# Optimization experiments

Measured on AMD Instinct MI355X. Metric: run time of the kernel, lower is better.

Reference implementation:

```python
import jax, jax.numpy as jnp
import numpy as np

N = 50000          # nodes
E = 800000         # edges (avg degree 16)
DIN, DH, DOUT = 128, 256, 40


def setup_inputs() -> dict:
    key = jax.random.key(0)
    ks = jax.random.split(key, 6)
    x = jax.random.normal(ks[0], (N, DIN), dtype=jnp.float32)
    edge_index = jax.random.randint(ks[1], (2, E), 0, N, dtype=jnp.int32)
    W1 = jax.random.normal(ks[2], (DIN, DH), dtype=jnp.float32) * (1.0 / np.sqrt(DIN))
    b1 = jnp.zeros((DH,), dtype=jnp.float32)
    W2 = jax.random.normal(ks[3], (DH, DOUT), dtype=jnp.float32) * (1.0 / np.sqrt(DH))
    b2 = jnp.zeros((DOUT,), dtype=jnp.float32)
    return {"x": x, "edge_index": edge_index, "W1": W1, "b1": b1, "W2": W2, "b2": b2}


def gcn_conv(x, src, dst, W, b, n):
    # PyG GCNConv: add self-loops, symmetric normalization D^-1/2 A D^-1/2,
    # dense projection, scatter-sum aggregation, then bias.
    deg = jax.ops.segment_sum(jnp.ones_like(dst, dtype=x.dtype), dst, num_segments=n)
    dinv = jnp.where(deg > 0, jax.lax.rsqrt(deg), 0.0)
    norm = dinv[src] * dinv[dst]          # [E+N]
    h = x @ W                              # [N, dout] dense GEMM
    msg = h[src] * norm[:, None]          # gather + scale, [E+N, dout]
    out = jax.ops.segment_sum(msg, dst, num_segments=n)  # scatter-add
    return out + b


def reference(x, edge_index, W1, b1, W2, b2):
    n = x.shape[0]
    loops = jnp.arange(n, dtype=edge_index.dtype)
    src = jnp.concatenate([edge_index[0], loops])
    dst = jnp.concatenate([edge_index[1], loops])
    h = jax.nn.relu(gcn_conv(x, src, dst, W1, b1, n))
    h = gcn_conv(h, src, dst, W2, b2, n)
    return jax.nn.log_softmax(h, axis=1)
```

## Files before the change

### kernel.cpp

```cpp
#include <hip/hip_runtime.h>
#include <math.h>

#define DIN 128
#define DH 256
#define DOUT 40
#define MLP_ROWS 64

#define BSH 7
#define BNODES 128
#define NBUK 391
#define CAP 4096
#define PART_T 512
#define PART_EPB 8
#define PART_CHUNK (PART_T * PART_EPB)

typedef short short8 __attribute__((ext_vector_type(8)));
typedef float f32x4 __attribute__((ext_vector_type(4)));

__device__ inline unsigned f2bf(float f) {
    unsigned u = __float_as_uint(f);
    return (u + 0x7fffu + ((u >> 16) & 1u)) >> 16;
}
__device__ inline float bflo(unsigned u) { return __uint_as_float(u << 16); }
__device__ inline float bfhi(unsigned u) { return __uint_as_float(u & 0xffff0000u); }

__global__ void k_prep(const float* __restrict__ W1, const float* __restrict__ W2,
                       unsigned* __restrict__ w1t, unsigned* __restrict__ w2t,
                       int* __restrict__ gcur) {
    int i = blockIdx.x * blockDim.x + threadIdx.x;
    if (i < 256 * 64) {
        int c = i >> 6;
        int kk = (i & 63) * 2;
        w1t[i] = f2bf(W1[kk * DH + c]) | (f2bf(W1[(kk + 1) * DH + c]) << 16);
        return;
    }
    i -= 256 * 64;
    if (i < 48 * 128) {
        int col = i >> 7;
        int kk = (i & 127) * 2;
        float a = (col < DOUT) ? W2[kk * DOUT + col] : 0.f;
        float bb = (col < DOUT) ? W2[(kk + 1) * DOUT + col] : 0.f;
        w2t[i] = f2bf(a) | (f2bf(bb) << 16);
        return;
    }
    i -= 48 * 128;
    if (i < NBUK) gcur[i] = i * CAP;
}

__global__ __launch_bounds__(PART_T) void k_partition(
    const int* __restrict__ src, const int* __restrict__ dst,
    int* __restrict__ gcur, unsigned* __restrict__ raw, int E) {
    __shared__ int hist[NBUK];
    __shared__ int lbase[NBUK];
    int tid = threadIdx.x;
    int base_e = blockIdx.x * PART_CHUNK;

    for (int i = tid; i < NBUK; i += PART_T) hist[i] = 0;
    __syncthreads();

    int s[PART_EPB], d[PART_EPB];
#pragma unroll
    for (int k = 0; k < PART_EPB; ++k) {
        int e = base_e + k * PART_T + tid;
        if (e < E) { s[k] = src[e]; d[k] = dst[e]; }
        else d[k] = -1;
    }
#pragma unroll
    for (int k = 0; k < PART_EPB; ++k)
        if (d[k] >= 0) atomicAdd(&hist[d[k] >> BSH], 1);
    __syncthreads();

    for (int b = tid; b < NBUK; b += PART_T) {
        int c = hist[b];
        lbase[b] = c ? atomicAdd(&gcur[b], c) : 0;
    }
    __syncthreads();
    for (int i = tid; i < NBUK; i += PART_T) hist[i] = 0;
    __syncthreads();

#pragma unroll
    for (int k = 0; k < PART_EPB; ++k) {
        if (d[k] >= 0) {
            int b = d[k] >> BSH;
            int pos = lbase[b] + atomicAdd(&hist[b], 1);
            if (pos < (b + 1) * CAP)
                raw[pos] = ((unsigned)(d[k] & (BNODES - 1)) << 16) | (unsigned)s[k];
        }
    }
}

__global__ __launch_bounds__(256) void k_bucket_csr(
    const unsigned* __restrict__ raw, const int* __restrict__ gcur,
    const float* __restrict__ x,
    int* __restrict__ row_ptr, int* __restrict__ row_end,
    float* __restrict__ dinv, unsigned short* __restrict__ esrc,
    unsigned* __restrict__ xb, int n) {
    __shared__ int cnt[BNODES];
    __shared__ int scn[BNODES];
    __shared__ int lcur[BNODES];
    __shared__ float sdinv[BNODES];
    int b = blockIdx.x;
    int tid = threadIdx.x;
    int base = b * CAP;
    int size = gcur[b] - base;
    if (size > CAP) size = CAP;

    if (tid < BNODES) cnt[tid] = 0;
    __syncthreads();
    for (int i = tid; i < size; i += 256)
        atomicAdd(&cnt[raw[base + i] >> 16], 1);
    __syncthreads();

    if (tid < BNODES) scn[tid] = (cnt[tid] + 7) & ~7;
    __syncthreads();
    for (int off = 1; off < BNODES; off <<= 1) {
        int v = 0;
        if (tid < BNODES && tid >= off) v = scn[tid - off];
        __syncthreads();
        if (tid < BNODES) scn[tid] += v;
        __syncthreads();
    }
    if (tid < BNODES) {
        int c8 = (cnt[tid] + 7) & ~7;
        int excl = scn[tid] - c8;
        if (excl > CAP) excl = CAP;
        int re = excl + cnt[tid];
        if (re > CAP) re = CAP;
        lcur[tid] = excl;
        float dv = rsqrtf((float)cnt[tid] + 1.0f);
        sdinv[tid] = dv;
        int g = b * BNODES + tid;
        if (g < n) {
            row_ptr[g] = base + excl;
            row_end[g] = base + re;
            dinv[g]    = dv;
        }
    }
    __syncthreads();
    for (int i = tid; i < size; i += 256) {
        unsigned rec = raw[base + i];
        int pos = atomicAdd(&lcur[rec >> 16], 1);
        if (pos < CAP) esrc[base + pos] = (unsigned short)(rec & 0xffffu);
    }
    int nloc = n - b * BNODES;
    if (nloc > BNODES) nloc = BNODES;
    for (int i = tid; i < nloc * 64; i += 256) {
        int local = i >> 6, c = i & 63;
        int g = b * BNODES + local;
        float dv = sdinv[local];
        float2 v = ((const float2*)x)[(size_t)g * 64 + c];
        xb[(size_t)g * 64 + c] = f2bf(dv * v.x) | (f2bf(dv * v.y) << 16);
    }
}

__global__ void k_gather_agg1(const uint2* __restrict__ xb2,
                              const unsigned short* __restrict__ esrc,
                              const int* __restrict__ row_ptr, const int* __restrict__ row_end,
                              const float* __restrict__ dinv, uint2* __restrict__ axb2, int n) {
    int wid = (blockIdx.x * blockDim.x + threadIdx.x) >> 6;
    int lane = threadIdx.x & 63;
    int node = wid * 2 + (lane >> 5);
    int hl = lane & 31;
    if (node >= n) return;
    int beg = row_ptr[node], end = row_end[node];
    uint2 sv = xb2[(size_t)node * 32 + hl];
    float ax = bflo(sv.x), ay = bfhi(sv.x);
    float az = bflo(sv.y), aw = bfhi(sv.y);
    int t = beg;
    for (; t + 8 <= end; t += 8) {
        uint4 q = *(const uint4*)(esrc + t);
        int s0 = q.x & 0xffff, s1 = q.x >> 16, s2 = q.y & 0xffff, s3 = q.y >> 16;
        int s4 = q.z & 0xffff, s5 = q.z >> 16, s6 = q.w & 0xffff, s7 = q.w >> 16;
        uint2 v0 = xb2[(size_t)s0 * 32 + hl], v1 = xb2[(size_t)s1 * 32 + hl];
        uint2 v2 = xb2[(size_t)s2 * 32 + hl], v3 = xb2[(size_t)s3 * 32 + hl];
        uint2 v4 = xb2[(size_t)s4 * 32 + hl], v5 = xb2[(size_t)s5 * 32 + hl];
        uint2 v6 = xb2[(size_t)s6 * 32 + hl], v7 = xb2[(size_t)s7 * 32 + hl];
        ax += bflo(v0.x) + bflo(v1.x) + bflo(v2.x) + bflo(v3.x)
            + bflo(v4.x) + bflo(v5.x) + bflo(v6.x) + bflo(v7.x);
        ay += bfhi(v0.x) + bfhi(v1.x) + bfhi(v2.x) + bfhi(v3.x)
            + bfhi(v4.x) + bfhi(v5.x) + bfhi(v6.x) + bfhi(v7.x);
        az += bflo(v0.y) + bflo(v1.y) + bflo(v2.y) + bflo(v3.y)
            + bflo(v4.y) + bflo(v5.y) + bflo(v6.y) + bflo(v7.y);
        aw += bfhi(v0.y) + bfhi(v1.y) + bfhi(v2.y) + bfhi(v3.y)
            + bfhi(v4.y) + bfhi(v5.y) + bfhi(v6.y) + bfhi(v7.y);
    }
    for (; t < end; ++t) {
        int s = esrc[t];
        uint2 v = xb2[(size_t)s * 32 + hl];
        ax += bflo(v.x); ay += bfhi(v.x);
        az += bflo(v.y); aw += bfhi(v.y);
    }
    float dn = dinv[node];
    ax *= dn; ay *= dn; az *= dn; aw *= dn;
    axb2[(size_t)node * 32 + hl] =
        make_uint2(f2bf(ax) | (f2bf(ay) << 16), f2bf(az) | (f2bf(aw) << 16));
}

__global__ __launch_bounds__(256) void k_mlp_mfma(
    const unsigned short* __restrict__ axb, const unsigned short* __restrict__ w1t,
    const float* __restrict__ b1, const unsigned short* __restrict__ w2t,
    const float* __restrict__ dinv, unsigned short* __restrict__ pb, int n) {
    __shared__ __align__(16) char smem[65536];
    const int tid = threadIdx.x;
    const int lane = tid & 63;
    const int wv = tid >> 6;
    const int l15 = lane & 15;
    const int lg = lane >> 4;
    const int blockRow = blockIdx.x * MLP_ROWS;

    for (int i = tid; i < 256 * 16; i += 256) {
        int j = i >> 4, seg = i & 15;
        short8 v = *(const short8*)(w1t + j * 128 + seg * 8);
        *(short8*)(smem + j * 256 + ((seg * 16) ^ ((j & 7) << 4))) = v;
    }

    int arow = blockRow + wv * 16 + l15;
    if (arow >= n) arow = n - 1;
    const unsigned short* axp = axb + (size_t)arow * DIN + lg * 8;
    short8 aF[4];
#pragma unroll
    for (int ks = 0; ks < 4; ++ks) aF[ks] = *(const short8*)(axp + ks * 32);

    __syncthreads();

    f32x4 acc[16];
#pragma unroll
    for (int nt = 0; nt < 16; ++nt) acc[nt] = (f32x4){0.f, 0.f, 0.f, 0.f};
#pragma unroll
    for (int ks = 0; ks < 4; ++ks) {
        int kb = (ks * 32 + lg * 8) * 2;
#pragma unroll
        for (int nt = 0; nt < 16; ++nt) {
            int j = nt * 16 + l15;
            short8 bF = *(const short8*)(smem + j * 256 + (kb ^ ((j & 7) << 4)));
            acc[nt] = __builtin_amdgcn_mfma_f32_16x16x32_bf16(aF[ks], bF, acc[nt], 0, 0, 0);
        }
    }
    __syncthreads();

    unsigned short* s_h = (unsigned short*)smem;
    unsigned short* s_w2 = (unsigned short*)(smem + 33792);

#pragma unroll
    for (int nt = 0; nt < 16; ++nt) {
        int col = nt * 16 + l15;
        float bias = b1[col];
#pragma unroll
        for (int r = 0; r < 4; ++r) {
            int row = wv * 16 + lg * 4 + r;
            float v = fmaxf(acc[nt][r] + bias, 0.f);
            s_h[row * 264 + col] = (unsigned short)f2bf(v);
        }
    }
    for (int i = tid; i < 48 * 32; i += 256) {
        int j = i >> 5, seg = i & 31;
        short8 v = *(const short8*)(w2t + j * 256 + seg * 8);
        *(short8*)(s_w2 + j * 264 + seg * 8) = v;
    }
    __syncthreads();

    f32x4 acc2[3];
#pragma unroll
    for (int t = 0; t < 3; ++t) acc2[t] = (f32x4){0.f, 0.f, 0.f, 0.f};
#pragma unroll
    for (int ks = 0; ks < 8; ++ks) {
        int k = ks * 32 + lg * 8;
        short8 aH = *(const short8*)(s_h + (wv * 16 + l15) * 264 + k);
#pragma unroll
        for (int t = 0; t < 3; ++t) {
            short8 bF = *(const short8*)(s_w2 + (t * 16 + l15) * 264 + k);
            acc2[t] = __builtin_amdgcn_mfma_f32_16x16x32_bf16(aH, bF, acc2[t], 0, 0, 0);
        }
    }
    float dnr[4];
#pragma unroll
    for (int r = 0; r < 4; ++r) {
        int row = blockRow + wv * 16 + lg * 4 + r;
        dnr[r] = (row < n) ? dinv[row] : 0.f;
    }
#pragma unroll
    for (int t = 0; t < 3; ++t) {
        int col = t * 16 + l15;
        if (col < DOUT) {
#pragma unroll
            for (int r = 0; r < 4; ++r) {
                int row = blockRow + wv * 16 + lg * 4 + r;
                if (row < n)
                    pb[(size_t)row * DOUT + col] = (unsigned short)f2bf(acc2[t][r] * dnr[r]);
            }
        }
    }
}

__global__ void k_gather2_lsm(const unsigned* __restrict__ pbu,
                              const unsigned short* __restrict__ esrc,
                              const int* __restrict__ row_ptr, const int* __restrict__ row_end,
                              const float* __restrict__ dinv, const float* __restrict__ b2,
                              float* __restrict__ out, int n) {
    int wid = (blockIdx.x * blockDim.x + threadIdx.x) >> 6;
    int lane = threadIdx.x & 63;
    int node = wid * 2 + (lane >> 5);
    int hl = lane & 31;
    if (node >= n) return;
    int beg = row_ptr[node], end = row_end[node];
    float dn = dinv[node];
    int cl = (hl < 20) ? hl : 0;
    unsigned pv = pbu[(size_t)node * 20 + cl];
    float accx = bflo(pv);
    float accy = bfhi(pv);
    int t = beg;
    for (; t + 8 <= end; t += 8) {
        uint4 q = *(const uint4*)(esrc + t);
        int s0 = q.x & 0xffff, s1 = q.x >> 16, s2 = q.y & 0xffff, s3 = q.y >> 16;
        int s4 = q.z & 0xffff, s5 = q.z >> 16, s6 = q.w & 0xffff, s7 = q.w >> 16;
        unsigned p0 = pbu[(size_t)s0 * 20 + cl], p1 = pbu[(size_t)s1 * 20 + cl];
        unsigned p2 = pbu[(size_t)s2 * 20 + cl], p3 = pbu[(size_t)s3 * 20 + cl];
        unsigned p4 = pbu[(size_t)s4 * 20 + cl], p5 = pbu[(size_t)s5 * 20 + cl];
        unsigned p6 = pbu[(size_t)s6 * 20 + cl], p7 = pbu[(size_t)s7 * 20 + cl];
        accx += bflo(p0) + bflo(p1) + bflo(p2) + bflo(p3)
              + bflo(p4) + bflo(p5) + bflo(p6) + bflo(p7);
        accy += bfhi(p0) + bfhi(p1) + bfhi(p2) + bfhi(p3)
              + bfhi(p4) + bfhi(p5) + bfhi(p6) + bfhi(p7);
    }
    for (; t < end; ++t) {
        int s = esrc[t];
        unsigned p = pbu[(size_t)s * 20 + cl];
        accx += bflo(p);
        accy += bfhi(p);
    }
    float vx = -INFINITY, vy = -INFINITY;
    if (hl < 20) {
        float2 bv = ((const float2*)b2)[hl];
        vx = dn * accx + bv.x;
        vy = dn * accy + bv.y;
    }
    float m = fmaxf(vx, vy);
#pragma unroll
    for (int off = 16; off; off >>= 1) m = fmaxf(m, __shfl_xor(m, off, 32));
    float ex = (hl < 20) ? (expf(vx - m) + expf(vy - m)) : 0.f;
    float ssum = ex;
#pragma unroll
    for (int off = 16; off; off >>= 1) ssum += __shfl_xor(ssum, off, 32);
    float ls = logf(ssum);
    if (hl < 20)
        ((float2*)(out + (size_t)node * DOUT))[hl] = make_float2(vx - m - ls, vy - m - ls);
}

extern "C" void kernel_launch(void* const* d_in, const int* in_sizes, int n_in,
                              void* d_out, int out_size, void* d_ws, size_t ws_size,
                              hipStream_t stream) {
    const float* x  = (const float*)d_in[0];
    const int*   ei = (const int*)d_in[1];
    const float* W1 = (const float*)d_in[2];
    const float* b1 = (const float*)d_in[3];
    const float* W2 = (const float*)d_in[4];
    const float* b2 = (const float*)d_in[5];
    float* out = (float*)d_out;

    int n = in_sizes[0] / DIN;
    int E = in_sizes[1] / 2;
    const int* src = ei;
    const int* dst = ei + E;

    int*            gcur    = (int*)d_ws;
    int*            row_ptr = gcur + 512;
    int*            row_end = row_ptr + n;
    float*          dinv    = (float*)(row_end + n);
    unsigned*       w1t     = (unsigned*)(dinv + n);
    unsigned*       w2t     = w1t + 16384;
    unsigned*       raw     = w2t + 6144;
    unsigned short* esrc    = (unsigned short*)(raw + (size_t)NBUK * CAP);
    unsigned*       xb      = (unsigned*)(esrc + (size_t)NBUK * CAP);
    unsigned*       axb     = xb + (size_t)n * 64;
    unsigned short* pb      = (unsigned short*)xb;

    const int B = 256;
    int part_blocks = (E + PART_CHUNK - 1) / PART_CHUNK;
    int prep_items = 256 * 64 + 48 * 128 + NBUK;
    int npairs = (n + 1) / 2;
    int gath_blocks = (int)(((size_t)npairs * 64 + B - 1) / B);

    k_prep<<<(prep_items + B - 1) / B, B, 0, stream>>>(W1, W2, w1t, w2t, gcur);
    k_partition<<<part_blocks, PART_T, 0, stream>>>(src, dst, gcur, raw, E);
    k_bucket_csr<<<NBUK, B, 0, stream>>>(raw, gcur, x, row_ptr, row_end, dinv, esrc, xb, n);
    k_gather_agg1<<<gath_blocks, B, 0, stream>>>(
        (const uint2*)xb, esrc, row_ptr, row_end, dinv, (uint2*)axb, n);
    k_mlp_mfma<<<(n + MLP_ROWS - 1) / MLP_ROWS, B, 0, stream>>>(
        (const unsigned short*)axb, (const unsigned short*)w1t, b1,
        (const unsigned short*)w2t, dinv, pb, n);
    k_gather2_lsm<<<gath_blocks, B, 0, stream>>>(
        (const unsigned*)pb, esrc, row_ptr, row_end, dinv, b2, out, n);
}
```

Measured before the change: 120.9 us.

## Fuse layer-1 aggregation into MLP kernel and fold weight prep into partition

The layer-1 neighbor gather now runs inside the MFMA MLP kernel. Each block aggregates its 64 rows straight into shared memory, so the intermediate aggregated feature buffer is no longer written to and reread from global memory, and one launch is saved. Weight conversion to bf16 is folded into the partition kernel, and bucket cursors are now relative and zeroed with a memset, which removes the separate prep kernel. W1 tiles are now read from global memory or cache instead of being staged in swizzled LDS. The fused kernel also gives each block a serial gather phase of eight nodes per wave-half, which may lower memory-level parallelism.

```diff
diff --git a/kernel.cpp b/kernel.cpp
--- a/kernel.cpp
+++ b/kernel.cpp
@@ -4,7 +4,6 @@
 #define DIN 128
 #define DH 256
 #define DOUT 40
-#define MLP_ROWS 64
 
 #define BSH 7
 #define BNODES 128
@@ -24,37 +23,32 @@
 __device__ inline float bflo(unsigned u) { return __uint_as_float(u << 16); }
 __device__ inline float bfhi(unsigned u) { return __uint_as_float(u & 0xffff0000u); }
 
-__global__ void k_prep(const float* __restrict__ W1, const float* __restrict__ W2,
-                       unsigned* __restrict__ w1t, unsigned* __restrict__ w2t,
-                       int* __restrict__ gcur) {
-    int i = blockIdx.x * blockDim.x + threadIdx.x;
-    if (i < 256 * 64) {
-        int c = i >> 6;
-        int kk = (i & 63) * 2;
-        w1t[i] = f2bf(W1[kk * DH + c]) | (f2bf(W1[(kk + 1) * DH + c]) << 16);
-        return;
-    }
-    i -= 256 * 64;
-    if (i < 48 * 128) {
-        int col = i >> 7;
-        int kk = (i & 127) * 2;
-        float a = (col < DOUT) ? W2[kk * DOUT + col] : 0.f;
-        float bb = (col < DOUT) ? W2[(kk + 1) * DOUT + col] : 0.f;
-        w2t[i] = f2bf(a) | (f2bf(bb) << 16);
-        return;
-    }
-    i -= 48 * 128;
-    if (i < NBUK) gcur[i] = i * CAP;
-}
-
-__global__ __launch_bounds__(PART_T) void k_partition(
+__global__ __launch_bounds__(PART_T) void k_part_prep(
     const int* __restrict__ src, const int* __restrict__ dst,
-    int* __restrict__ gcur, unsigned* __restrict__ raw, int E) {
+    const float* __restrict__ W1, const float* __restrict__ W2,
+    int* __restrict__ gcur, unsigned* __restrict__ raw,
+    unsigned* __restrict__ w1t, unsigned* __restrict__ w2t, int E) {
     __shared__ int hist[NBUK];
     __shared__ int lbase[NBUK];
     int tid = threadIdx.x;
+
+    int prep_items = 256 * 64 + 48 * 128;
+    for (int i = blockIdx.x * PART_T + tid; i < prep_items; i += gridDim.x * PART_T) {
+        if (i < 256 * 64) {
+            int c = i >> 6;
+            int kk = (i & 63) * 2;
+            w1t[i] = f2bf(W1[kk * DH + c]) | (f2bf(W1[(kk + 1) * DH + c]) << 16);
+        } else {
+            int j = i - 256 * 64;
+            int col = j >> 7;
+            int kk = (j & 127) * 2;
+            float a = (col < DOUT) ? W2[kk * DOUT + col] : 0.f;
+            float bb = (col < DOUT) ? W2[(kk + 1) * DOUT + col] : 0.f;
+            w2t[j] = f2bf(a) | (f2bf(bb) << 16);
+        }
+    }
+
     int base_e = blockIdx.x * PART_CHUNK;
-
     for (int i = tid; i < NBUK; i += PART_T) hist[i] = 0;
     __syncthreads();
 
@@ -72,7 +66,7 @@
 
     for (int b = tid; b < NBUK; b += PART_T) {
         int c = hist[b];
-        lbase[b] = c ? atomicAdd(&gcur[b], c) : 0;
+        lbase[b] = b * CAP + (c ? atomicAdd(&gcur[b], c) : 0);
     }
     __syncthreads();
     for (int i = tid; i < NBUK; i += PART_T) hist[i] = 0;
@@ -102,7 +96,7 @@
     int b = blockIdx.x;
     int tid = threadIdx.x;
     int base = b * CAP;
-    int size = gcur[b] - base;
+    int size = gcur[b];
     if (size > CAP) size = CAP;
 
     if (tid < BNODES) cnt[tid] = 0;
@@ -153,74 +147,66 @@
     }
 }
 
-__global__ void k_gather_agg1(const uint2* __restrict__ xb2,
-                              const unsigned short* __restrict__ esrc,
-                              const int* __restrict__ row_ptr, const int* __restrict__ row_end,
-                              const float* __restrict__ dinv, uint2* __restrict__ axb2, int n) {
-    int wid = (blockIdx.x * blockDim.x + threadIdx.x) >> 6;
-    int lane = threadIdx.x & 63;
-    int node = wid * 2 + (lane >> 5);
-    int hl = lane & 31;
-    if (node >= n) return;
-    int beg = row_ptr[node], end = row_end[node];
-    uint2 sv = xb2[(size_t)node * 32 + hl];
-    float ax = bflo(sv.x), ay = bfhi(sv.x);
-    float az = bflo(sv.y), aw = bfhi(sv.y);
-    int t = beg;
-    for (; t + 8 <= end; t += 8) {
-        uint4 q = *(const uint4*)(esrc + t);
-        int s0 = q.x & 0xffff, s1 = q.x >> 16, s2 = q.y & 0xffff, s3 = q.y >> 16;
-        int s4 = q.z & 0xffff, s5 = q.z >> 16, s6 = q.w & 0xffff, s7 = q.w >> 16;
-        uint2 v0 = xb2[(size_t)s0 * 32 + hl], v1 = xb2[(size_t)s1 * 32 + hl];
-        uint2 v2 = xb2[(size_t)s2 * 32 + hl], v3 = xb2[(size_t)s3 * 32 + hl];
-        uint2 v4 = xb2[(size_t)s4 * 32 + hl], v5 = xb2[(size_t)s5 * 32 + hl];
-        uint2 v6 = xb2[(size_t)s6 * 32 + hl], v7 = xb2[(size_t)s7 * 32 + hl];
-        ax += bflo(v0.x) + bflo(v1.x) + bflo(v2.x) + bflo(v3.x)
-            + bflo(v4.x) + bflo(v5.x) + bflo(v6.x) + bflo(v7.x);
-        ay += bfhi(v0.x) + bfhi(v1.x) + bfhi(v2.x) + bfhi(v3.x)
-            + bfhi(v4.x) + bfhi(v5.x) + bfhi(v6.x) + bfhi(v7.x);
-        az += bflo(v0.y) + bflo(v1.y) + bflo(v2.y) + bflo(v3.y)
-            + bflo(v4.y) + bflo(v5.y) + bflo(v6.y) + bflo(v7.y);
-        aw += bfhi(v0.y) + bfhi(v1.y) + bfhi(v2.y) + bfhi(v3.y)
-            + bfhi(v4.y) + bfhi(v5.y) + bfhi(v6.y) + bfhi(v7.y);
-    }
-    for (; t < end; ++t) {
-        int s = esrc[t];
-        uint2 v = xb2[(size_t)s * 32 + hl];
-        ax += bflo(v.x); ay += bfhi(v.x);
-        az += bflo(v.y); aw += bfhi(v.y);
-    }
-    float dn = dinv[node];
-    ax *= dn; ay *= dn; az *= dn; aw *= dn;
-    axb2[(size_t)node * 32 + hl] =
-        make_uint2(f2bf(ax) | (f2bf(ay) << 16), f2bf(az) | (f2bf(aw) << 16));
-}
-
-__global__ __launch_bounds__(256) void k_mlp_mfma(
-    const unsigned short* __restrict__ axb, const unsigned short* __restrict__ w1t,
+__global__ __launch_bounds__(256) void k_agg_mlp(
+    const uint2* __restrict__ xb2, const unsigned short* __restrict__ esrc,
+    const int* __restrict__ row_ptr, const int* __restrict__ row_end,
+    const float* __restrict__ dinv, const unsigned short* __restrict__ w1t,
     const float* __restrict__ b1, const unsigned short* __restrict__ w2t,
-    const float* __restrict__ dinv, unsigned short* __restrict__ pb, int n) {
-    __shared__ __align__(16) char smem[65536];
+    unsigned short* __restrict__ pb, int n) {
+    __shared__ __align__(16) unsigned short s_h[64][264];
+    __shared__ __align__(16) unsigned short s_w2[48][264];
     const int tid = threadIdx.x;
     const int lane = tid & 63;
     const int wv = tid >> 6;
     const int l15 = lane & 15;
     const int lg = lane >> 4;
-    const int blockRow = blockIdx.x * MLP_ROWS;
-
-    for (int i = tid; i < 256 * 16; i += 256) {
-        int j = i >> 4, seg = i & 15;
-        short8 v = *(const short8*)(w1t + j * 128 + seg * 8);
-        *(short8*)(smem + j * 256 + ((seg * 16) ^ ((j & 7) << 4))) = v;
-    }
-
-    int arow = blockRow + wv * 16 + l15;
-    if (arow >= n) arow = n - 1;
-    const unsigned short* axp = axb + (size_t)arow * DIN + lg * 8;
+    const int hl = lane & 31;
+    const int half = lane >> 5;
+    const int blockRow = blockIdx.x * 64;
+
+    for (int p = 0; p < 8; ++p) {
+        int rlocal = wv * 16 + p * 2 + half;
+        int node = blockRow + rlocal;
+        float ax = 0.f, ay = 0.f, az = 0.f, aw = 0.f;
+        if (node < n) {
+            int beg = row_ptr[node], end = row_end[node];
+            uint2 sv = xb2[(size_t)node * 32 + hl];
+            ax = bflo(sv.x); ay = bfhi(sv.x); az = bflo(sv.y); aw = bfhi(sv.y);
+            int t = beg;
+            for (; t + 8 <= end; t += 8) {
+                uint4 q = *(const uint4*)(esrc + t);
+                int s0 = q.x & 0xffff, s1 = q.x >> 16, s2 = q.y & 0xffff, s3 = q.y >> 16;
+                int s4 = q.z & 0xffff, s5 = q.z >> 16, s6 = q.w & 0xffff, s7 = q.w >> 16;
+                uint2 v0 = xb2[(size_t)s0 * 32 + hl], v1 = xb2[(size_t)s1 * 32 + hl];
+                uint2 v2 = xb2[(size_t)s2 * 32 + hl], v3 = xb2[(size_t)s3 * 32 + hl];
+                uint2 v4 = xb2[(size_t)s4 * 32 + hl], v5 = xb2[(size_t)s5 * 32 + hl];
+                uint2 v6 = xb2[(size_t)s6 * 32 + hl], v7 = xb2[(size_t)s7 * 32 + hl];
+                ax += bflo(v0.x) + bflo(v1.x) + bflo(v2.x) + bflo(v3.x)
+                    + bflo(v4.x) + bflo(v5.x) + bflo(v6.x) + bflo(v7.x);
+                ay += bfhi(v0.x) + bfhi(v1.x) + bfhi(v2.x) + bfhi(v3.x)
+                    + bfhi(v4.x) + bfhi(v5.x) + bfhi(v6.x) + bfhi(v7.x);
+                az += bflo(v0.y) + bflo(v1.y) + bflo(v2.y) + bflo(v3.y)
+                    + bflo(v4.y) + bflo(v5.y) + bflo(v6.y) + bflo(v7.y);
+                aw += bfhi(v0.y) + bfhi(v1.y) + bfhi(v2.y) + bfhi(v3.y)
+                    + bfhi(v4.y) + bfhi(v5.y) + bfhi(v6.y) + bfhi(v7.y);
+            }
+            for (; t < end; ++t) {
+                int s = esrc[t];
+                uint2 v = xb2[(size_t)s * 32 + hl];
+                ax += bflo(v.x); ay += bfhi(v.x);
+                az += bflo(v.y); aw += bfhi(v.y);
+            }
+            float dn = dinv[node];
+            ax *= dn; ay *= dn; az *= dn; aw *= dn;
+        }
+        *(uint2*)&s_h[rlocal][hl * 4] =
+            make_uint2(f2bf(ax) | (f2bf(ay) << 16), f2bf(az) | (f2bf(aw) << 16));
+    }
+
     short8 aF[4];
 #pragma unroll
-    for (int ks = 0; ks < 4; ++ks) aF[ks] = *(const short8*)(axp + ks * 32);
-
+    for (int ks = 0; ks < 4; ++ks)
+        aF[ks] = *(const short8*)&s_h[wv * 16 + l15][ks * 32 + lg * 8];
     __syncthreads();
 
     f32x4 acc[16];
@@ -228,18 +214,13 @@
     for (int nt = 0; nt < 16; ++nt) acc[nt] = (f32x4){0.f, 0.f, 0.f, 0.f};
 #pragma unroll
     for (int ks = 0; ks < 4; ++ks) {
-        int kb = (ks * 32 + lg * 8) * 2;
 #pragma unroll
         for (int nt = 0; nt < 16; ++nt) {
             int j = nt * 16 + l15;
-            short8 bF = *(const short8*)(smem + j * 256 + (kb ^ ((j & 7) << 4)));
+            short8 bF = *(const short8*)(w1t + (size_t)j * 128 + ks * 32 + lg * 8);
             acc[nt] = __builtin_amdgcn_mfma_f32_16x16x32_bf16(aF[ks], bF, acc[nt], 0, 0, 0);
         }
     }
-    __syncthreads();
-
-    unsigned short* s_h = (unsigned short*)smem;
-    unsigned short* s_w2 = (unsigned short*)(smem + 33792);
 
 #pragma unroll
     for (int nt = 0; nt < 16; ++nt) {
@@ -249,13 +230,13 @@
         for (int r = 0; r < 4; ++r) {
             int row = wv * 16 + lg * 4 + r;
             float v = fmaxf(acc[nt][r] + bias, 0.f);
-            s_h[row * 264 + col] = (unsigned short)f2bf(v);
+            s_h[row][col] = (unsigned short)f2bf(v);
         }
     }
     for (int i = tid; i < 48 * 32; i += 256) {
         int j = i >> 5, seg = i & 31;
         short8 v = *(const short8*)(w2t + j * 256 + seg * 8);
-        *(short8*)(s_w2 + j * 264 + seg * 8) = v;
+        *(short8*)&s_w2[j][seg * 8] = v;
     }
     __syncthreads();
 
@@ -265,10 +246,10 @@
 #pragma unroll
     for (int ks = 0; ks < 8; ++ks) {
         int k = ks * 32 + lg * 8;
-        short8 aH = *(const short8*)(s_h + (wv * 16 + l15) * 264 + k);
+        short8 aH = *(const short8*)&s_h[wv * 16 + l15][k];
 #pragma unroll
         for (int t = 0; t < 3; ++t) {
-            short8 bF = *(const short8*)(s_w2 + (t * 16 + l15) * 264 + k);
+            short8 bF = *(const short8*)&s_w2[t * 16 + l15][k];
             acc2[t] = __builtin_amdgcn_mfma_f32_16x16x32_bf16(aH, bF, acc2[t], 0, 0, 0);
         }
     }
@@ -371,23 +352,20 @@
     unsigned*       raw     = w2t + 6144;
     unsigned short* esrc    = (unsigned short*)(raw + (size_t)NBUK * CAP);
     unsigned*       xb      = (unsigned*)(esrc + (size_t)NBUK * CAP);
-    unsigned*       axb     = xb + (size_t)n * 64;
-    unsigned short* pb      = (unsigned short*)xb;
+    unsigned short* pb      = (unsigned short*)(xb + (size_t)n * 64);
 
     const int B = 256;
     int part_blocks = (E + PART_CHUNK - 1) / PART_CHUNK;
-    int prep_items = 256 * 64 + 48 * 128 + NBUK;
     int npairs = (n + 1) / 2;
     int gath_blocks = (int)(((size_t)npairs * 64 + B - 1) / B);
 
-    k_prep<<<(prep_items + B - 1) / B, B, 0, stream>>>(W1, W2, w1t, w2t, gcur);
-    k_partition<<<part_blocks, PART_T, 0, stream>>>(src, dst, gcur, raw, E);
+    hipMemsetAsync(gcur, 0, NBUK * sizeof(int), stream);
+    k_part_prep<<<part_blocks, PART_T, 0, stream>>>(
+        src, dst, W1, W2, gcur, raw, w1t, w2t, E);
     k_bucket_csr<<<NBUK, B, 0, stream>>>(raw, gcur, x, row_ptr, row_end, dinv, esrc, xb, n);
-    k_gather_agg1<<<gath_blocks, B, 0, stream>>>(
-        (const uint2*)xb, esrc, row_ptr, row_end, dinv, (uint2*)axb, n);
-    k_mlp_mfma<<<(n + MLP_ROWS - 1) / MLP_ROWS, B, 0, stream>>>(
-        (const unsigned short*)axb, (const unsigned short*)w1t, b1,
-        (const unsigned short*)w2t, dinv, pb, n);
+    k_agg_mlp<<<(n + 63) / 64, B, 0, stream>>>(
+        (const uint2*)xb, esrc, row_ptr, row_end, dinv,
+        (const unsigned short*)w1t, b1, (const unsigned short*)w2t, pb, n);
     k_gather2_lsm<<<gath_blocks, B, 0, stream>>>(
         (const unsigned*)pb, esrc, row_ptr, row_end, dinv, b2, out, n);
 }
```

Result: slower. 176.9 us (+46.4%).
